# Kernel optimization log

Measured on AMD Instinct MI355X. Metric: run time of the kernel, lower is better.

Reference implementation:

```python
import jax, jax.numpy as jnp
import numpy as np

C = 10.0  # init kwarg


def _per_sample(g, dx, dy, sx, sy):
    # g: [2, h, w]; dx, dy, sx, sy scalars
    h, w = g.shape[1], g.shape[2]
    dy1f = jnp.floor(dy)
    dx1f = jnp.floor(dx)
    dy1 = dy1f.astype(jnp.int32)
    dx1 = dx1f.astype(jnp.int32)
    fy = dy - dy1f  # dy - dy1_f
    fx = dx - dx1f  # dx - dx1_f
    w22 = fx * fy
    w21 = fx * (1.0 - fy)
    w12 = (1.0 - fx) * fy
    w11 = (1.0 - fx) * (1.0 - fy)

    # S(ro, co)[c, i, j] == g[c, i+ro, j+co]  (wrapped; wrap region is masked out)
    S = lambda ro, co: jnp.roll(g, (-ro, -co), axis=(1, 2))

    # dx > 0 branch: delta(i,j) = g[i,j] - bilinear(g at (i+dy, j+dx))
    d_pos = g - (w22 * S(dy1 + 1, dx1 + 1) + w21 * S(dy1, dx1 + 1)
                 + w12 * S(dy1 + 1, dx1) + w11 * S(dy1, dx1))

    # dx <= 0 branch (faithful to the original index pattern):
    #   fx-weighted terms anchor at g[i+dy2, j+1], (1-fx)-weighted at g[i+dy2, j];
    #   sampled terms at rows i (fy) / i+1 (1-fy), column j - dx1.
    a2 = S(dy1 + 1, 1)
    a1 = S(dy1 + 1, 0)
    s_top = S(0, -dx1)
    s_bot = S(1, -dx1)
    d_neg = (w22 * (a2 - s_top) + w21 * (a2 - s_bot)
             + w12 * (a1 - s_top) + w11 * (a1 - s_bot))

    pos = dx > 0
    delta = jnp.where(pos, d_pos, d_neg)  # [2, h, w]

    ii = jnp.arange(h, dtype=jnp.int32)[:, None]
    jj = jnp.arange(w, dtype=jnp.int32)[None, :]
    rows = h - dy1 - 1                      # valid rows in both branches
    cols = jnp.where(pos, w - dx1 - 1, w + dx1)
    mask = (ii < rows) & (jj < cols)        # [h, w]
    count = (rows * cols).astype(g.dtype)

    val = delta[0] * sy + delta[1] * sx
    return jnp.sum(jnp.where(mask, val * val, jnp.zeros((), g.dtype))) / count


def setup_inputs() -> dict:
    key = jax.random.key(0)
    k1, k2, k3 = jax.random.split(key, 3)
    B, h, w = 32, 512, 512
    grid = jax.random.normal(k1, (B, 2, h, w), jnp.float32)
    u = jax.random.uniform(k2, (B, 3), jnp.float32)
    sign = jnp.where(u[:, 0] < 0.5, -1.0, 1.0)
    gt_x = sign * (0.2 + 0.3 * u[:, 1])   # dx = -C*gt_x -> |dx| in (2,5), both signs
    gt_y = 0.05 + 0.5 * u[:, 2]           # dy = C*gt_y in (0.5, 5.5)
    gt_sym_axis = jnp.stack([gt_x, gt_y], axis=1)
    gd_sym_axis = jax.random.normal(k3, (B, 2), jnp.float32)
    return {"grid": grid, "gt_sym_axis": gt_sym_axis, "gd_sym_axis": gd_sym_axis}


def reference(grid, gt_sym_axis, gd_sym_axis):
    dxs = -C * gt_sym_axis[:, 0]
    dys = C * gt_sym_axis[:, 1]
    losses = jax.vmap(_per_sample)(grid, dxs, dys,
                                   gd_sym_axis[:, 0], gd_sym_axis[:, 1])
    return jnp.mean(losses)
```

## Files before the change

kernel.cpp:

```cpp
#include <hip/hip_runtime.h>


#define GH 512
#define GW 512
#define GB 32
#define ROWS_PER_BLOCK 8
#define BLOCK 256
#define NBLK_X ((GH + ROWS_PER_BLOCK - 1) / ROWS_PER_BLOCK)
#define NPART (NBLK_X * GB)

__global__ __launch_bounds__(BLOCK) void bilinear_sym_loss_stage1(
    const float* __restrict__ grid,
    const float* __restrict__ gt,
    const float* __restrict__ gd,
    float* __restrict__ partials)
{
    const int b = blockIdx.z;

    const float dx = -10.0f * gt[b * 2 + 0];
    const float dy =  10.0f * gt[b * 2 + 1];
    const float sx = gd[b * 2 + 0];
    const float sy = gd[b * 2 + 1];

    const float dy1f = floorf(dy);
    const float dx1f = floorf(dx);
    const int dy1 = (int)dy1f;
    const int dx1 = (int)dx1f;
    const float fy = dy - dy1f;
    const float fx = dx - dx1f;

    const bool pos = dx > 0.0f;
    const int rows = GH - dy1 - 1;
    const int cols = pos ? (GW - dx1 - 1) : (GW + dx1);

    const float w22 = fx * fy;
    const float w21 = fx * (1.0f - fy);
    const float w12 = (1.0f - fx) * fy;
    const float w11 = (1.0f - fx) * (1.0f - fy);

    const float* __restrict__ g0 = grid + (size_t)b * 2u * GH * GW;
    const float* __restrict__ g1 = g0 + GH * GW;

    const int tid = threadIdx.x;
    const int row0 = blockIdx.x * ROWS_PER_BLOCK;

    float acc = 0.0f;

    for (int r = 0; r < ROWS_PER_BLOCK; ++r) {
        const int i = row0 + r;
        if (i >= rows) break;

        if (pos) {
            const float* r0c  = g0 + i * GW;
            const float* r0a  = g0 + (i + dy1) * GW + dx1;
            const float* r0b  = g0 + (i + dy1 + 1) * GW + dx1;
            const float* r1c  = g1 + i * GW;
            const float* r1a  = g1 + (i + dy1) * GW + dx1;
            const float* r1b  = g1 + (i + dy1 + 1) * GW + dx1;
            for (int j = tid; j < cols; j += BLOCK) {
                float interp0 = w11 * r0a[j];
                interp0 = fmaf(w21, r0a[j + 1], interp0);
                interp0 = fmaf(w12, r0b[j], interp0);
                interp0 = fmaf(w22, r0b[j + 1], interp0);
                const float d0 = r0c[j] - interp0;

                float interp1 = w11 * r1a[j];
                interp1 = fmaf(w21, r1a[j + 1], interp1);
                interp1 = fmaf(w12, r1b[j], interp1);
                interp1 = fmaf(w22, r1b[j + 1], interp1);
                const float d1 = r1c[j] - interp1;

                const float val = fmaf(d0, sy, d1 * sx);
                acc = fmaf(val, val, acc);
            }
        } else {
            const float omfx = 1.0f - fx;
            const float omfy = 1.0f - fy;
            const int jo = -dx1;
            const float* r0a = g0 + (i + dy1 + 1) * GW;
            const float* r0t = g0 + i * GW + jo;
            const float* r0s = g0 + (i + 1) * GW + jo;
            const float* r1a = g1 + (i + dy1 + 1) * GW;
            const float* r1t = g1 + i * GW + jo;
            const float* r1s = g1 + (i + 1) * GW + jo;
            for (int j = tid; j < cols; j += BLOCK) {
                float d0 = fx * r0a[j + 1];
                d0 = fmaf(omfx, r0a[j], d0);
                d0 = fmaf(-fy, r0t[j], d0);
                d0 = fmaf(-omfy, r0s[j], d0);

                float d1 = fx * r1a[j + 1];
                d1 = fmaf(omfx, r1a[j], d1);
                d1 = fmaf(-fy, r1t[j], d1);
                d1 = fmaf(-omfy, r1s[j], d1);

                const float val = fmaf(d0, sy, d1 * sx);
                acc = fmaf(val, val, acc);
            }
        }
    }

    for (int off = 32; off > 0; off >>= 1)
        acc += __shfl_down(acc, off, 64);

    __shared__ float wave_sums[BLOCK / 64];
    const int lane = tid & 63;
    const int wid = tid >> 6;
    if (lane == 0) wave_sums[wid] = acc;
    __syncthreads();

    if (tid == 0) {
        float s = wave_sums[0] + wave_sums[1] + wave_sums[2] + wave_sums[3];
        const float count = (float)rows * (float)cols;
        const float scale = 1.0f / (count * (float)GB);
        partials[b * NBLK_X + blockIdx.x] = s * scale;
    }
}

__global__ __launch_bounds__(BLOCK) void bilinear_sym_loss_stage2(
    const float* __restrict__ partials,
    float* __restrict__ out)
{
    const int tid = threadIdx.x;
    float acc = 0.0f;
    for (int i = tid; i < NPART; i += BLOCK)
        acc += partials[i];

    for (int off = 32; off > 0; off >>= 1)
        acc += __shfl_down(acc, off, 64);

    __shared__ float wave_sums[BLOCK / 64];
    const int lane = tid & 63;
    const int wid = tid >> 6;
    if (lane == 0) wave_sums[wid] = acc;
    __syncthreads();

    if (tid == 0)
        out[0] = wave_sums[0] + wave_sums[1] + wave_sums[2] + wave_sums[3];
}

extern "C" void kernel_launch(void* const* d_in, const int* in_sizes, int n_in,
                              void* d_out, int out_size, void* d_ws, size_t ws_size,
                              hipStream_t stream) {
    const float* grid = (const float*)d_in[0];
    const float* gt   = (const float*)d_in[1];
    const float* gd   = (const float*)d_in[2];
    float* out = (float*)d_out;
    float* partials = (float*)d_ws;

    dim3 grid1(NBLK_X, 1, GB);
    bilinear_sym_loss_stage1<<<grid1, dim3(BLOCK), 0, stream>>>(grid, gt, gd, partials);
    bilinear_sym_loss_stage2<<<dim3(1), dim3(BLOCK), 0, stream>>>(partials, out);
}
```

Baseline: 107.2 us.

## Vectorize loads to four columns per thread and split block across two rows

Each thread now processes four consecutive columns using float4 loads (aligned for the center/anchor row, unaligned struct loads for shifted rows), plus a scalar tail, and the 256-thread block is split into two 128-thread halves working on different rows at once. The branch on dx sign is hoisted outside the row loop. This aims to cut load instruction count and reuse neighbouring values across adjacent output columns, at the cost of possibly misaligned wide loads and more registers.

```diff
diff --git a/kernel.cpp b/kernel.cpp
--- a/kernel.cpp
+++ b/kernel.cpp
@@ -4,10 +4,60 @@
 #define GH 512
 #define GW 512
 #define GB 32
+#define CH (GH * GW)
 #define ROWS_PER_BLOCK 8
 #define BLOCK 256
 #define NBLK_X ((GH + ROWS_PER_BLOCK - 1) / ROWS_PER_BLOCK)
 #define NPART (NBLK_X * GB)
+
+struct F4U { float x, y, z, w; };
+
+__device__ __forceinline__ F4U ld4u(const float* p) {
+    return *(const F4U*)p;
+}
+
+__device__ __forceinline__ void interp4_pos(
+    const float* __restrict__ rc, const float* __restrict__ ra,
+    const float* __restrict__ rb, int j0,
+    float w11, float w21, float w12, float w22, float d[4])
+{
+    const float4 c = *(const float4*)(rc + j0);
+    const F4U A = ld4u(ra + j0);
+    const float a4 = ra[j0 + 4];
+    const F4U Bv = ld4u(rb + j0);
+    const float b4 = rb[j0 + 4];
+
+    float t;
+    t = w11 * A.x; t = fmaf(w21, A.y, t); t = fmaf(w12, Bv.x, t); t = fmaf(w22, Bv.y, t);
+    d[0] = c.x - t;
+    t = w11 * A.y; t = fmaf(w21, A.z, t); t = fmaf(w12, Bv.y, t); t = fmaf(w22, Bv.z, t);
+    d[1] = c.y - t;
+    t = w11 * A.z; t = fmaf(w21, A.w, t); t = fmaf(w12, Bv.z, t); t = fmaf(w22, Bv.w, t);
+    d[2] = c.z - t;
+    t = w11 * A.w; t = fmaf(w21, a4, t);  t = fmaf(w12, Bv.w, t); t = fmaf(w22, b4, t);
+    d[3] = c.w - t;
+}
+
+__device__ __forceinline__ void interp4_neg(
+    const float* __restrict__ ra, const float* __restrict__ rt,
+    const float* __restrict__ rs, int j0,
+    float fx, float omfx, float fy, float omfy, float d[4])
+{
+    const float4 A = *(const float4*)(ra + j0);
+    const float a4 = ra[j0 + 4];
+    const F4U T = ld4u(rt + j0);
+    const F4U S = ld4u(rs + j0);
+
+    float t;
+    t = fx * A.y; t = fmaf(omfx, A.x, t); t = fmaf(-fy, T.x, t); t = fmaf(-omfy, S.x, t);
+    d[0] = t;
+    t = fx * A.z; t = fmaf(omfx, A.y, t); t = fmaf(-fy, T.y, t); t = fmaf(-omfy, S.y, t);
+    d[1] = t;
+    t = fx * A.w; t = fmaf(omfx, A.z, t); t = fmaf(-fy, T.z, t); t = fmaf(-omfy, S.z, t);
+    d[2] = t;
+    t = fx * a4;  t = fmaf(omfx, A.w, t); t = fmaf(-fy, T.w, t); t = fmaf(-omfy, S.w, t);
+    d[3] = t;
+}
 
 __global__ __launch_bounds__(BLOCK) void bilinear_sym_loss_stage1(
     const float* __restrict__ grid,
@@ -32,69 +82,100 @@
     const bool pos = dx > 0.0f;
     const int rows = GH - dy1 - 1;
     const int cols = pos ? (GW - dx1 - 1) : (GW + dx1);
+    const int ng4 = cols >> 2;
+    const int rem = cols & 3;
+    const int jt0 = ng4 << 2;
 
     const float w22 = fx * fy;
     const float w21 = fx * (1.0f - fy);
     const float w12 = (1.0f - fx) * fy;
     const float w11 = (1.0f - fx) * (1.0f - fy);
-
-    const float* __restrict__ g0 = grid + (size_t)b * 2u * GH * GW;
-    const float* __restrict__ g1 = g0 + GH * GW;
+    const float omfx = 1.0f - fx;
+    const float omfy = 1.0f - fy;
+
+    const float* __restrict__ g0 = grid + (size_t)b * 2u * CH;
 
     const int tid = threadIdx.x;
+    const int g = tid & 127;
+    const int half = tid >> 7;
     const int row0 = blockIdx.x * ROWS_PER_BLOCK;
 
     float acc = 0.0f;
 
-    for (int r = 0; r < ROWS_PER_BLOCK; ++r) {
-        const int i = row0 + r;
-        if (i >= rows) break;
-
-        if (pos) {
-            const float* r0c  = g0 + i * GW;
-            const float* r0a  = g0 + (i + dy1) * GW + dx1;
-            const float* r0b  = g0 + (i + dy1 + 1) * GW + dx1;
-            const float* r1c  = g1 + i * GW;
-            const float* r1a  = g1 + (i + dy1) * GW + dx1;
-            const float* r1b  = g1 + (i + dy1 + 1) * GW + dx1;
-            for (int j = tid; j < cols; j += BLOCK) {
-                float interp0 = w11 * r0a[j];
-                interp0 = fmaf(w21, r0a[j + 1], interp0);
-                interp0 = fmaf(w12, r0b[j], interp0);
-                interp0 = fmaf(w22, r0b[j + 1], interp0);
-                const float d0 = r0c[j] - interp0;
-
-                float interp1 = w11 * r1a[j];
-                interp1 = fmaf(w21, r1a[j + 1], interp1);
-                interp1 = fmaf(w12, r1b[j], interp1);
-                interp1 = fmaf(w22, r1b[j + 1], interp1);
-                const float d1 = r1c[j] - interp1;
-
-                const float val = fmaf(d0, sy, d1 * sx);
+    if (pos) {
+        for (int rp = 0; rp < ROWS_PER_BLOCK; rp += 2) {
+            const int i = row0 + rp + half;
+            if (i >= rows) continue;
+
+            const float* r0c = g0 + i * GW;
+            const float* r0a = g0 + (i + dy1) * GW + dx1;
+            const float* r0b = r0a + GW;
+            const float* r1c = r0c + CH;
+            const float* r1a = r0a + CH;
+            const float* r1b = r0b + CH;
+
+            if (g < ng4) {
+                const int j0 = g << 2;
+                float d0[4], d1[4];
+                interp4_pos(r0c, r0a, r0b, j0, w11, w21, w12, w22, d0);
+                interp4_pos(r1c, r1a, r1b, j0, w11, w21, w12, w22, d1);
+                #pragma unroll
+                for (int k = 0; k < 4; ++k) {
+                    const float val = fmaf(d0[k], sy, d1[k] * sx);
+                    acc = fmaf(val, val, acc);
+                }
+            }
+            if (g < rem) {
+                const int j = jt0 + g;
+                float t0 = w11 * r0a[j];
+                t0 = fmaf(w21, r0a[j + 1], t0);
+                t0 = fmaf(w12, r0b[j], t0);
+                t0 = fmaf(w22, r0b[j + 1], t0);
+                const float e0 = r0c[j] - t0;
+                float t1 = w11 * r1a[j];
+                t1 = fmaf(w21, r1a[j + 1], t1);
+                t1 = fmaf(w12, r1b[j], t1);
+                t1 = fmaf(w22, r1b[j + 1], t1);
+                const float e1 = r1c[j] - t1;
+                const float val = fmaf(e0, sy, e1 * sx);
                 acc = fmaf(val, val, acc);
             }
-        } else {
-            const float omfx = 1.0f - fx;
-            const float omfy = 1.0f - fy;
-            const int jo = -dx1;
+        }
+    } else {
+        const int jo = -dx1;
+        for (int rp = 0; rp < ROWS_PER_BLOCK; rp += 2) {
+            const int i = row0 + rp + half;
+            if (i >= rows) continue;
+
             const float* r0a = g0 + (i + dy1 + 1) * GW;
             const float* r0t = g0 + i * GW + jo;
-            const float* r0s = g0 + (i + 1) * GW + jo;
-            const float* r1a = g1 + (i + dy1 + 1) * GW;
-            const float* r1t = g1 + i * GW + jo;
-            const float* r1s = g1 + (i + 1) * GW + jo;
-            for (int j = tid; j < cols; j += BLOCK) {
-                float d0 = fx * r0a[j + 1];
-                d0 = fmaf(omfx, r0a[j], d0);
-                d0 = fmaf(-fy, r0t[j], d0);
-                d0 = fmaf(-omfy, r0s[j], d0);
-
-                float d1 = fx * r1a[j + 1];
-                d1 = fmaf(omfx, r1a[j], d1);
-                d1 = fmaf(-fy, r1t[j], d1);
-                d1 = fmaf(-omfy, r1s[j], d1);
-
-                const float val = fmaf(d0, sy, d1 * sx);
+            const float* r0s = r0t + GW;
+            const float* r1a = r0a + CH;
+            const float* r1t = r0t + CH;
+            const float* r1s = r0s + CH;
+
+            if (g < ng4) {
+                const int j0 = g << 2;
+                float d0[4], d1[4];
+                interp4_neg(r0a, r0t, r0s, j0, fx, omfx, fy, omfy, d0);
+                interp4_neg(r1a, r1t, r1s, j0, fx, omfx, fy, omfy, d1);
+                #pragma unroll
+                for (int k = 0; k < 4; ++k) {
+                    const float val = fmaf(d0[k], sy, d1[k] * sx);
+                    acc = fmaf(val, val, acc);
+                }
+            }
+            if (g < rem) {
+                const int j = jt0 + g;
+                float e0 = fx * r0a[j + 1];
+                e0 = fmaf(omfx, r0a[j], e0);
+                e0 = fmaf(-fy, r0t[j], e0);
+                e0 = fmaf(-omfy, r0s[j], e0);
+                float e1 = fx * r1a[j + 1];
+                e1 = fmaf(omfx, r1a[j], e1);
+                e1 = fmaf(-fy, r1t[j], e1);
+                e1 = fmaf(-omfy, r1s[j], e1);
+                const float val = fmaf(e0, sy, e1 * sx);
                 acc = fmaf(val, val, acc);
             }
         }
```

Result: faster. 102.3 us (-4.5%).

## Register-tile 8 columns by 4 rows per thread with vector loads and row reuse

Applied to the files above, without the earlier changes.

Each thread now handles 8 consecutive columns across 4 rows. It loads them with 16-byte vector loads and carries the previous row's values in registers, so each row is not re-read. This cuts the number of global load instructions and the redundant row fetches that the per-element loop had, and doubles the rows per block. The tail columns are handled by shifting the last tile left and masking the duplicated elements. The cost is higher register pressure, unaligned vector loads when dx1 is odd, and fewer blocks overall.

```diff
diff --git a/kernel.cpp b/kernel.cpp
--- a/kernel.cpp
+++ b/kernel.cpp
@@ -4,10 +4,28 @@
 #define GH 512
 #define GW 512
 #define GB 32
-#define ROWS_PER_BLOCK 8
+#define CH (GH * GW)
+#define RPB 16
 #define BLOCK 256
-#define NBLK_X ((GH + ROWS_PER_BLOCK - 1) / ROWS_PER_BLOCK)
+#define NBLK_X (GH / RPB)
 #define NPART (NBLK_X * GB)
+
+struct F4U { float x, y, z, w; };
+
+__device__ __forceinline__ void load9(const float* __restrict__ p, float* o) {
+    const F4U a = *(const F4U*)p;
+    const F4U b = *(const F4U*)(p + 4);
+    o[0]=a.x; o[1]=a.y; o[2]=a.z; o[3]=a.w;
+    o[4]=b.x; o[5]=b.y; o[6]=b.z; o[7]=b.w;
+    o[8] = p[8];
+}
+
+__device__ __forceinline__ void load8(const float* __restrict__ p, float* o) {
+    const F4U a = *(const F4U*)p;
+    const F4U b = *(const F4U*)(p + 4);
+    o[0]=a.x; o[1]=a.y; o[2]=a.z; o[3]=a.w;
+    o[4]=b.x; o[5]=b.y; o[6]=b.z; o[7]=b.w;
+}
 
 __global__ __launch_bounds__(BLOCK) void bilinear_sym_loss_stage1(
     const float* __restrict__ grid,
@@ -15,7 +33,7 @@
     const float* __restrict__ gd,
     float* __restrict__ partials)
 {
-    const int b = blockIdx.z;
+    const int b = blockIdx.y;
 
     const float dx = -10.0f * gt[b * 2 + 0];
     const float dy =  10.0f * gt[b * 2 + 1];
@@ -33,69 +51,95 @@
     const int rows = GH - dy1 - 1;
     const int cols = pos ? (GW - dx1 - 1) : (GW + dx1);
 
+    const float omfx = 1.0f - fx;
+    const float omfy = 1.0f - fy;
     const float w22 = fx * fy;
-    const float w21 = fx * (1.0f - fy);
-    const float w12 = (1.0f - fx) * fy;
-    const float w11 = (1.0f - fx) * (1.0f - fy);
+    const float w21 = fx * omfy;
+    const float w12 = omfx * fy;
+    const float w11 = omfx * omfy;
 
-    const float* __restrict__ g0 = grid + (size_t)b * 2u * GH * GW;
-    const float* __restrict__ g1 = g0 + GH * GW;
+    const float* __restrict__ g0 = grid + (size_t)b * 2u * CH;
 
     const int tid = threadIdx.x;
-    const int row0 = blockIdx.x * ROWS_PER_BLOCK;
+    const int cc = tid & 63;
+    const int rg = tid >> 6;
+    const int i0 = blockIdx.x * RPB + rg * 4;
+
+    int j0 = cc << 3;
+    int kmin = 0;
+    if (j0 > cols - 8) { kmin = j0 - (cols - 8); j0 = cols - 8; }
 
     float acc = 0.0f;
 
-    for (int r = 0; r < ROWS_PER_BLOCK; ++r) {
-        const int i = row0 + r;
-        if (i >= rows) break;
-
-        if (pos) {
-            const float* r0c  = g0 + i * GW;
-            const float* r0a  = g0 + (i + dy1) * GW + dx1;
-            const float* r0b  = g0 + (i + dy1 + 1) * GW + dx1;
-            const float* r1c  = g1 + i * GW;
-            const float* r1a  = g1 + (i + dy1) * GW + dx1;
-            const float* r1b  = g1 + (i + dy1 + 1) * GW + dx1;
-            for (int j = tid; j < cols; j += BLOCK) {
-                float interp0 = w11 * r0a[j];
-                interp0 = fmaf(w21, r0a[j + 1], interp0);
-                interp0 = fmaf(w12, r0b[j], interp0);
-                interp0 = fmaf(w22, r0b[j + 1], interp0);
-                const float d0 = r0c[j] - interp0;
-
-                float interp1 = w11 * r1a[j];
-                interp1 = fmaf(w21, r1a[j + 1], interp1);
-                interp1 = fmaf(w12, r1b[j], interp1);
-                interp1 = fmaf(w22, r1b[j + 1], interp1);
-                const float d1 = r1c[j] - interp1;
-
-                const float val = fmaf(d0, sy, d1 * sx);
-                acc = fmaf(val, val, acc);
+    if (pos) {
+        if (i0 < rows) {
+            const float* pa0 = g0 + (i0 + dy1) * GW + dx1 + j0;
+            const float* pc0 = g0 + i0 * GW + j0;
+            float P0[9], P1[9];
+            load9(pa0, P0);
+            load9(pa0 + CH, P1);
+            #pragma unroll
+            for (int r = 0; r < 4; ++r) {
+                const int i = i0 + r;
+                if (i >= rows) break;
+                float B0[9], B1[9], C0[8], C1[8];
+                load9(pa0 + (r + 1) * GW, B0);
+                load9(pa0 + (r + 1) * GW + CH, B1);
+                load8(pc0 + r * GW, C0);
+                load8(pc0 + r * GW + CH, C1);
+                #pragma unroll
+                for (int k = 0; k < 8; ++k) {
+                    float t0 = w11 * P0[k];
+                    t0 = fmaf(w21, P0[k + 1], t0);
+                    t0 = fmaf(w12, B0[k], t0);
+                    t0 = fmaf(w22, B0[k + 1], t0);
+                    const float d0 = C0[k] - t0;
+                    float t1 = w11 * P1[k];
+                    t1 = fmaf(w21, P1[k + 1], t1);
+                    t1 = fmaf(w12, B1[k], t1);
+                    t1 = fmaf(w22, B1[k + 1], t1);
+                    const float d1 = C1[k] - t1;
+                    float v = fmaf(d0, sy, d1 * sx);
+                    v = (k >= kmin) ? v : 0.0f;
+                    acc = fmaf(v, v, acc);
+                }
+                #pragma unroll
+                for (int k = 0; k < 9; ++k) { P0[k] = B0[k]; P1[k] = B1[k]; }
             }
-        } else {
-            const float omfx = 1.0f - fx;
-            const float omfy = 1.0f - fy;
+        }
+    } else {
+        if (i0 < rows) {
             const int jo = -dx1;
-            const float* r0a = g0 + (i + dy1 + 1) * GW;
-            const float* r0t = g0 + i * GW + jo;
-            const float* r0s = g0 + (i + 1) * GW + jo;
-            const float* r1a = g1 + (i + dy1 + 1) * GW;
-            const float* r1t = g1 + i * GW + jo;
-            const float* r1s = g1 + (i + 1) * GW + jo;
-            for (int j = tid; j < cols; j += BLOCK) {
-                float d0 = fx * r0a[j + 1];
-                d0 = fmaf(omfx, r0a[j], d0);
-                d0 = fmaf(-fy, r0t[j], d0);
-                d0 = fmaf(-omfy, r0s[j], d0);
-
-                float d1 = fx * r1a[j + 1];
-                d1 = fmaf(omfx, r1a[j], d1);
-                d1 = fmaf(-fy, r1t[j], d1);
-                d1 = fmaf(-omfy, r1s[j], d1);
-
-                const float val = fmaf(d0, sy, d1 * sx);
-                acc = fmaf(val, val, acc);
+            const float* pt0 = g0 + i0 * GW + jo + j0;
+            const float* pa0 = g0 + (i0 + dy1 + 1) * GW + j0;
+            float T0[8], T1[8];
+            load8(pt0, T0);
+            load8(pt0 + CH, T1);
+            #pragma unroll
+            for (int r = 0; r < 4; ++r) {
+                const int i = i0 + r;
+                if (i >= rows) break;
+                float S0[8], S1[8], A0[9], A1[9];
+                load8(pt0 + (r + 1) * GW, S0);
+                load8(pt0 + (r + 1) * GW + CH, S1);
+                load9(pa0 + r * GW, A0);
+                load9(pa0 + r * GW + CH, A1);
+                #pragma unroll
+                for (int k = 0; k < 8; ++k) {
+                    float d0 = fx * A0[k + 1];
+                    d0 = fmaf(omfx, A0[k], d0);
+                    d0 = fmaf(-fy, T0[k], d0);
+                    d0 = fmaf(-omfy, S0[k], d0);
+                    float d1 = fx * A1[k + 1];
+                    d1 = fmaf(omfx, A1[k], d1);
+                    d1 = fmaf(-fy, T1[k], d1);
+                    d1 = fmaf(-omfy, S1[k], d1);
+                    float v = fmaf(d0, sy, d1 * sx);
+                    v = (k >= kmin) ? v : 0.0f;
+                    acc = fmaf(v, v, acc);
+                }
+                #pragma unroll
+                for (int k = 0; k < 8; ++k) { T0[k] = S0[k]; T1[k] = S1[k]; }
             }
         }
     }
@@ -110,7 +154,7 @@
     __syncthreads();
 
     if (tid == 0) {
-        float s = wave_sums[0] + wave_sums[1] + wave_sums[2] + wave_sums[3];
+        const float s = wave_sums[0] + wave_sums[1] + wave_sums[2] + wave_sums[3];
         const float count = (float)rows * (float)cols;
         const float scale = 1.0f / (count * (float)GB);
         partials[b * NBLK_X + blockIdx.x] = s * scale;
@@ -148,7 +192,7 @@
     float* out = (float*)d_out;
     float* partials = (float*)d_ws;
 
-    dim3 grid1(NBLK_X, 1, GB);
+    dim3 grid1(NBLK_X, GB);
     bilinear_sym_loss_stage1<<<grid1, dim3(BLOCK), 0, stream>>>(grid, gt, gd, partials);
     bilinear_sym_loss_stage2<<<dim3(1), dim3(BLOCK), 0, stream>>>(partials, out);
 }
```

Result: faster. 99.02 us, median of 2 (-7.6%).
